# Kernel tuning notes

Measured on AMD Instinct MI355X. Metric: run time of the kernel, lower is better.

The kernel has to match this reference:

```python
import jax, jax.numpy as jnp
import numpy as np

N_PER_G = 100  # nodes per graph


def setup_inputs() -> dict:
    key = jax.random.key(0)
    ks = jax.random.split(key, 12)
    N, G, E = 100000, 1000, 1600000
    ninp, nout, K, H, H2 = 3, 10, 5, 64, 32
    x = jax.random.normal(ks[0], (N, ninp), jnp.float32)
    # within-graph random edges (contiguous node blocks per graph)
    epg = E // G
    gid = jnp.arange(E, dtype=jnp.int32) // epg
    src = jax.random.randint(ks[1], (E,), 0, N_PER_G, jnp.int32) + gid * N_PER_G
    dst = jax.random.randint(ks[2], (E,), 0, N_PER_G, jnp.int32) + gid * N_PER_G
    edge_index = jnp.stack([src, dst])
    batch = (jnp.arange(N, dtype=jnp.int32) // N_PER_G)
    lambda_max = 1.5 + 0.5 * jax.random.uniform(ks[3], (G,), jnp.float32)
    s = 0.05
    W1 = jax.random.normal(ks[4], (K, ninp, H), jnp.float32) * s
    b1 = jnp.zeros((H,), jnp.float32)
    W2 = jax.random.normal(ks[5], (K, H, H), jnp.float32) * s
    b2 = jnp.zeros((H,), jnp.float32)
    W3 = jax.random.normal(ks[6], (K, H, H), jnp.float32) * s
    b3 = jnp.zeros((H,), jnp.float32)
    bn_gamma = jnp.ones((H,), jnp.float32)
    bn_beta = jnp.zeros((H,), jnp.float32)
    bn_mean = jnp.zeros((H,), jnp.float32)
    bn_var = jnp.ones((H,), jnp.float32)
    fc1_w = jax.random.normal(ks[7], (H, H2), jnp.float32) * s
    fc1_b = jnp.zeros((H2,), jnp.float32)
    fc2_w = jax.random.normal(ks[8], (H2, nout), jnp.float32) * s
    fc2_b = jnp.zeros((nout,), jnp.float32)
    return dict(x=x, edge_index=edge_index, batch=batch, lambda_max=lambda_max,
                W1=W1, b1=b1, W2=W2, b2=b2, W3=W3, b3=b3,
                bn_gamma=bn_gamma, bn_beta=bn_beta, bn_mean=bn_mean, bn_var=bn_var,
                fc1_w=fc1_w, fc1_b=fc1_b, fc2_w=fc2_w, fc2_b=fc2_b)


def _cheb_conv(x, W, b, row, col, coef_edge, coef_loop):
    # PyG ChebConv with sym-normalized scaled Laplacian:
    # Lhat x = scatter_add(coef_edge * x[col] -> row) + coef_loop * x
    N = x.shape[0]
    def lhat(h):
        return jax.ops.segment_sum(coef_edge[:, None] * h[col], row,
                                   num_segments=N) + coef_loop[:, None] * h
    Tx0 = x
    out = Tx0 @ W[0]
    Tx1 = lhat(x)
    out = out + Tx1 @ W[1]
    for k in range(2, W.shape[0]):
        Tx2 = 2.0 * lhat(Tx1) - Tx0
        out = out + Tx2 @ W[k]
        Tx0, Tx1 = Tx1, Tx2
    return out + b


def reference(x, edge_index, batch, lambda_max,
              W1, b1, W2, b2, W3, b3,
              bn_gamma, bn_beta, bn_mean, bn_var,
              fc1_w, fc1_b, fc2_w, fc2_b):
    N = x.shape[0]
    G = lambda_max.shape[0]
    row, col = edge_index[0], edge_index[1]
    # sym Laplacian normalization, scaled by 2/lambda_max (per-graph)
    deg = jax.ops.segment_sum(jnp.ones_like(row, dtype=x.dtype), row, num_segments=N)
    dis = jnp.where(deg > 0, deg, 1.0) ** -0.5
    dis = jnp.where(deg > 0, dis, 0.0)
    lmax_e = lambda_max[batch[row]]
    coef_edge = -(2.0 / lmax_e) * dis[row] * dis[col]   # off-diagonal of Lhat
    coef_loop = 2.0 / lambda_max[batch] - 1.0           # diagonal of Lhat
    h = jax.nn.relu(_cheb_conv(x, W1, b1, row, col, coef_edge, coef_loop))
    h = jax.nn.relu(_cheb_conv(h, W2, b2, row, col, coef_edge, coef_loop))
    h = jax.nn.relu(_cheb_conv(h, W3, b3, row, col, coef_edge, coef_loop))
    # global mean pool over graphs
    sums = jax.ops.segment_sum(h, batch, num_segments=G)
    cnts = jax.ops.segment_sum(jnp.ones((N,), h.dtype), batch, num_segments=G)
    g = sums / jnp.maximum(cnts, 1.0)[:, None]
    # BatchNorm1d (eval mode, running stats), eps=1e-5
    g = (g - bn_mean) * jax.lax.rsqrt(bn_var + 1e-5) * bn_gamma + bn_beta
    g = jax.nn.relu(g @ fc1_w + fc1_b)
    return jax.nn.log_softmax(g @ fc2_w + fc2_b, axis=1)
```

## Files before the change

### kernel.cpp

```cpp
#include <hip/hip_runtime.h>

#define NPG 100
#define HF 64
#define ST 72
#define SAT 136
#define CMW 29

typedef float  f4   __attribute__((ext_vector_type(4)));
typedef float  f16v __attribute__((ext_vector_type(16)));
typedef short  bf8  __attribute__((ext_vector_type(8)));

#define SZ_TC  (HF * SAT * 2)
#define SZ_TRM (128 * ST * 2)
#define OFF_TRM (2 * SZ_TC)
#define OFF_MISC (OFF_TRM + 2 * SZ_TRM)
#define SMEM_BYTES (OFF_MISC + 1280)

#define WT_TOTAL 46080

__device__ __forceinline__ unsigned short f2bf(float f) {
    unsigned u = __float_as_uint(f);
    u += 0x7fffu + ((u >> 16) & 1u);
    return (unsigned short)(u >> 16);
}
__device__ __forceinline__ unsigned cvt_pk_bf16(float lo, float hi) {
    unsigned r;
    asm("v_cvt_pk_bf16_f32 %0, %1, %2" : "=v"(r) : "v"(lo), "v"(hi));
    return r;
}
__device__ __forceinline__ f16v zerov16() {
    f16v z;
    #pragma unroll
    for (int i = 0; i < 16; i++) z[i] = 0.f;
    return z;
}
__device__ __forceinline__ void bar_lgkm() {
    asm volatile("s_waitcnt lgkmcnt(0)" ::: "memory");
    __builtin_amdgcn_s_barrier();
    __builtin_amdgcn_sched_barrier(0);
}

union BF8U { unsigned u[4]; bf8 b; };

__global__ void wconv(const float* __restrict__ W1, const float* __restrict__ W2,
                      const float* __restrict__ W3, unsigned short* __restrict__ ws)
{
    int idx = blockIdx.x * 256 + threadIdx.x;
    if (idx >= WT_TOTAL) return;
    float v;
    if (idx < 5120) {
        int k5 = idx >> 10, rem = idx & 1023, fo = rem >> 4, fi = rem & 15;
        v = (fi < 3) ? W1[(k5 * 3 + fi) * HF + fo] : 0.f;
    } else if (idx < 25600) {
        int j = idx - 5120;
        int k5 = j >> 12, rem = j & 4095, fo = rem >> 6, fi = rem & 63;
        v = W2[(k5 * HF + fi) * HF + fo];
    } else {
        int j = idx - 25600;
        int k5 = j >> 12, rem = j & 4095, fo = rem >> 6, fi = rem & 63;
        v = W3[(k5 * HF + fi) * HF + fo];
    }
    ws[idx] = f2bf(v);
}

__launch_bounds__(256, 2)
__global__ void chebreg(const float* __restrict__ x, const int* __restrict__ ei,
                        const float* __restrict__ lambda_max,
                        const unsigned short* __restrict__ Wt,
                        const float* __restrict__ b1, const float* __restrict__ b2,
                        const float* __restrict__ b3,
                        const float* __restrict__ bng, const float* __restrict__ bnb,
                        const float* __restrict__ bnm, const float* __restrict__ bnv,
                        const float* __restrict__ fc1w, const float* __restrict__ fc1b,
                        const float* __restrict__ fc2w, const float* __restrict__ fc2b,
                        float* __restrict__ out, int E_total, int epg)
{
    extern __shared__ char sm[];
    const int tid = threadIdx.x;
    const int g = blockIdx.x;
    const int ebase = g * epg, nbase = g * NPG;
    const int wg = tid >> 6, lane = tid & 63;
    const int l31 = lane & 31, hh = lane >> 5;
    const int ht  = wg & 1;
    const int Mt0 = (wg >> 1) * 2;
    const int fo  = ht * 32 + l31;

    unsigned* Cm  = (unsigned*)sm;
    float* dis    = (float*)(sm + OFF_MISC);
    float* pool   = (float*)(sm + OFF_MISC + 448);
    float* gvn    = (float*)(sm + OFF_MISC + 704);
    float* zf     = (float*)(sm + OFF_MISC + 960);
    float* logits = (float*)(sm + OFF_MISC + 1088);
    float* lsep   = (float*)(sm + OFF_MISC + 1152);

    const float lam = lambda_max[g];
    const float two_l = 2.0f / lam;
    const float cl = two_l - 1.0f;

    for (int i = tid; i < (128 * CMW) / 4; i += 256)
        ((f4*)Cm)[i] = (f4){0.f, 0.f, 0.f, 0.f};
    bar_lgkm();
    for (int e = tid; e < epg; e += 256) {
        int r = ei[ebase + e] - nbase;
        int c = ei[E_total + ebase + e] - nbase;
        atomicAdd(&Cm[r * CMW + (c >> 2)], 1u << (8 * (c & 3)));
    }
    bar_lgkm();
    if (tid < 112) {
        float dv = 0.f;
        if (tid < NPG) {
            unsigned s = 0;
            #pragma unroll
            for (int w = 0; w < 25; w++) {
                unsigned u = Cm[tid * CMW + w];
                s += (u & 255) + ((u >> 8) & 255) + ((u >> 16) & 255) + (u >> 24);
            }
            dv = s > 0 ? rsqrtf((float)s) : 0.f;
        }
        dis[tid] = dv;
    }
    bar_lgkm();

    bf8 af[2][7];
    #pragma unroll
    for (int m = 0; m < 2; m++) {
        int rr = 32 * (Mt0 + m) + l31;
        bool rv = (rr < NPG);
        float base = rv ? (-two_l * dis[rr]) : 0.f;
        #pragma unroll
        for (int Ks = 0; Ks < 7; Ks++) {
            int k0 = Ks * 16 + 8 * hh;
            unsigned w0 = rv ? Cm[rr * CMW + (k0 >> 2)]     : 0u;
            unsigned w1 = rv ? Cm[rr * CMW + (k0 >> 2) + 1] : 0u;
            float vv[8];
            #pragma unroll
            for (int j = 0; j < 8; j++) {
                int k = k0 + j;
                unsigned cnt = (((j < 4) ? w0 : w1) >> (8 * (k & 3))) & 255u;
                float v = base * (float)cnt * dis[k];
                if (rv && k == rr) v += cl;
                vv[j] = v;
            }
            BF8U t;
            #pragma unroll
            for (int p = 0; p < 4; p++) t.u[p] = cvt_pk_bf16(vv[2 * p], vv[2 * p + 1]);
            af[m][Ks] = t.b;
        }
    }
    bar_lgkm();

    for (int i = tid; i < SZ_TC / 16; i += 256)
        ((f4*)sm)[i] = (f4){0.f, 0.f, 0.f, 0.f};
    for (int i = tid; i < SZ_TRM / 16; i += 256)
        ((f4*)(sm + OFF_TRM))[i] = (f4){0.f, 0.f, 0.f, 0.f};
    if (tid < HF) pool[tid] = 0.f;
    bar_lgkm();
    if (tid < NPG) {
        unsigned short h0 = f2bf(x[(nbase + tid) * 3 + 0]);
        unsigned short h1 = f2bf(x[(nbase + tid) * 3 + 1]);
        unsigned short h2 = f2bf(x[(nbase + tid) * 3 + 2]);
        *(unsigned*)(sm + OFF_TRM + (tid * ST) * 2) = (unsigned)h0 | ((unsigned)h1 << 16);
        *(unsigned short*)(sm + OFF_TRM + (tid * ST + 2) * 2) = h2;
        *(unsigned short*)(sm + (0 * SAT + tid) * 2) = h0;
        *(unsigned short*)(sm + (1 * SAT + tid) * 2) = h1;
        *(unsigned short*)(sm + (2 * SAT + tid) * 2) = h2;
    }
    bar_lgkm();

    f16v acc[2];
    unsigned prev[2][8], oldr[2][8];
    const float* bsv[3] = {b1, b2, b3};

    for (int L = 0; L < 3; L++) {
        const bool l1 = (L == 0);
        const unsigned short* Wl = l1 ? Wt : (Wt + (L == 1 ? 5120 : 25600));
        const int pb = L & 1;
        const float bias = bsv[L][fo];
        acc[0] = zerov16();
        acc[1] = zerov16();

        if (L == 0) {
            #pragma unroll
            for (int m = 0; m < 2; m++) {
                unsigned short tv[16];
                #pragma unroll
                for (int r = 0; r < 16; r++) {
                    int np = (Mt0 + m) * 32 + (r & 3) + 8 * (r >> 2) + 4 * hh;
                    tv[r] = *(const unsigned short*)(sm + OFF_TRM + (np * ST + fo) * 2);
                }
                #pragma unroll
                for (int p = 0; p < 8; p++)
                    prev[m][p] = (unsigned)tv[2 * p] | ((unsigned)tv[2 * p + 1] << 16);
            }
        }

        auto TW = [&](int k5, const char* trb) {
            const int nKs = l1 ? 1 : 4;
            for (int Ks = 0; Ks < nKs; Ks++) {
                bf8 bw;
                if (l1) bw = *(const bf8*)(Wl + (k5 * 64 + fo) * 16 + 8 * hh);
                else    bw = *(const bf8*)(Wl + (k5 * 64 + fo) * 64 + Ks * 16 + 8 * hh);
                #pragma unroll
                for (int m = 0; m < 2; m++) {
                    bf8 a = *(const bf8*)(trb +
                              (((Mt0 + m) * 32 + l31) * ST + Ks * 16 + 8 * hh) * 2);
                    acc[m] = __builtin_amdgcn_mfma_f32_32x32x16_bf16(a, bw, acc[m], 0, 0, 0);
                }
            }
        };

        for (int s = 1; s <= 4; s++) {
            const int rp = (pb + s - 1) & 1, wp = rp ^ 1;
            const char* tcR = sm + rp * SZ_TC;
            const char* trR = sm + OFF_TRM + rp * SZ_TRM;
            char* tcW = sm + wp * SZ_TC;
            char* trW = sm + OFF_TRM + wp * SZ_TRM;

            TW(s - 1, trR);

            bf8 bfr[7];
            #pragma unroll
            for (int Ks = 0; Ks < 7; Ks++)
                bfr[Ks] = *(const bf8*)(tcR + (fo * SAT + Ks * 16 + 8 * hh) * 2);

            #pragma unroll
            for (int m = 0; m < 2; m++) {
                f16v c = zerov16();
                #pragma unroll
                for (int Ks = 0; Ks < 7; Ks++)
                    c = __builtin_amdgcn_mfma_f32_32x32x16_bf16(af[m][Ks], bfr[Ks], c, 0, 0, 0);
                #pragma unroll
                for (int p = 0; p < 8; p++) {
                    float ve = c[2 * p], vo = c[2 * p + 1];
                    if (s >= 2) {
                        unsigned o = oldr[m][p];
                        ve = 2.f * ve - __uint_as_float(o << 16);
                        vo = 2.f * vo - __uint_as_float(o & 0xffff0000u);
                    }
                    oldr[m][p] = prev[m][p];
                    prev[m][p] = cvt_pk_bf16(ve, vo);
                }
                if (s < 4) {
                    #pragma unroll
                    for (int q4 = 0; q4 < 4; q4++) {
                        int np0 = (Mt0 + m) * 32 + 8 * q4 + 4 * hh;
                        uint2 pk;
                        pk.x = prev[m][2 * q4];
                        pk.y = prev[m][2 * q4 + 1];
                        *(uint2*)(tcW + (fo * SAT + np0) * 2) = pk;
                    }
                }
                #pragma unroll
                for (int p = 0; p < 8; p++) {
                    int r0 = 2 * p;
                    int npb = (Mt0 + m) * 32 + (r0 & 3) + 8 * (r0 >> 2) + 4 * hh;
                    char* ad = trW + (npb * ST + fo) * 2;
                    *(unsigned short*)ad = (unsigned short)prev[m][p];
                    *(unsigned short*)(ad + ST * 2) = (unsigned short)(prev[m][p] >> 16);
                }
            }
            bar_lgkm();
        }

        TW(4, sm + OFF_TRM + pb * SZ_TRM);

        if (L < 2) {
            const int op = pb ^ 1;
            char* tcW = sm + op * SZ_TC;
            char* trW = sm + OFF_TRM + op * SZ_TRM;
            #pragma unroll
            for (int m = 0; m < 2; m++) {
                #pragma unroll
                for (int p = 0; p < 8; p++) {
                    float ve = fmaxf(acc[m][2 * p]     + bias, 0.f);
                    float vo = fmaxf(acc[m][2 * p + 1] + bias, 0.f);
                    prev[m][p] = cvt_pk_bf16(ve, vo);
                }
                #pragma unroll
                for (int q4 = 0; q4 < 4; q4++) {
                    int np0 = (Mt0 + m) * 32 + 8 * q4 + 4 * hh;
                    uint2 pk;
                    pk.x = prev[m][2 * q4];
                    pk.y = prev[m][2 * q4 + 1];
                    *(uint2*)(tcW + (fo * SAT + np0) * 2) = pk;
                }
                #pragma unroll
                for (int p = 0; p < 8; p++) {
                    int r0 = 2 * p;
                    int npb = (Mt0 + m) * 32 + (r0 & 3) + 8 * (r0 >> 2) + 4 * hh;
                    char* ad = trW + (npb * ST + fo) * 2;
                    *(unsigned short*)ad = (unsigned short)prev[m][p];
                    *(unsigned short*)(ad + ST * 2) = (unsigned short)(prev[m][p] >> 16);
                }
            }
            bar_lgkm();
        } else {
            float ssum = 0.f;
            #pragma unroll
            for (int m = 0; m < 2; m++) {
                #pragma unroll
                for (int r = 0; r < 16; r++) {
                    int np = (Mt0 + m) * 32 + (r & 3) + 8 * (r >> 2) + 4 * hh;
                    float h = fmaxf(acc[m][r] + bias, 0.f);
                    if (np < NPG) ssum += h;
                }
            }
            ssum += __shfl_xor(ssum, 32, 64);
            if (hh == 0) atomicAdd(&pool[fo], ssum);
            bar_lgkm();
        }
    }

    if (tid < HF) {
        float gv = pool[tid] * (1.0f / NPG);
        gv = (gv - bnm[tid]) * rsqrtf(bnv[tid] + 1e-5f) * bng[tid] + bnb[tid];
        gvn[tid] = gv;
    }
    bar_lgkm();
    if (tid < 32) {
        float a = fc1b[tid];
        for (int f = 0; f < HF; f++) a += gvn[f] * fc1w[f * 32 + tid];
        zf[tid] = fmaxf(a, 0.f);
    }
    bar_lgkm();
    if (tid < 10) {
        float a = fc2b[tid];
        for (int k = 0; k < 32; k++) a += zf[k] * fc2w[k * 10 + tid];
        logits[tid] = a;
    }
    bar_lgkm();
    if (tid == 0) {
        float m = logits[0];
        for (int i = 1; i < 10; i++) m = fmaxf(m, logits[i]);
        float s = 0.f;
        for (int i = 0; i < 10; i++) s += expf(logits[i] - m);
        lsep[0] = m + logf(s);
    }
    bar_lgkm();
    if (tid < 10) out[g * 10 + tid] = logits[tid] - lsep[0];
}

extern "C" void kernel_launch(void* const* d_in, const int* in_sizes, int n_in,
                              void* d_out, int out_size, void* d_ws, size_t ws_size,
                              hipStream_t stream) {
    const float* x    = (const float*)d_in[0];
    const int*   ei   = (const int*)d_in[1];
    const float* lmax = (const float*)d_in[3];
    const float* W1   = (const float*)d_in[4];
    const float* b1   = (const float*)d_in[5];
    const float* W2   = (const float*)d_in[6];
    const float* b2   = (const float*)d_in[7];
    const float* W3   = (const float*)d_in[8];
    const float* b3   = (const float*)d_in[9];
    const float* bng  = (const float*)d_in[10];
    const float* bnb  = (const float*)d_in[11];
    const float* bnm  = (const float*)d_in[12];
    const float* bnv  = (const float*)d_in[13];
    const float* fc1w = (const float*)d_in[14];
    const float* fc1b = (const float*)d_in[15];
    const float* fc2w = (const float*)d_in[16];
    const float* fc2b = (const float*)d_in[17];

    const int E = in_sizes[1] / 2;
    const int G = in_sizes[3];
    const int epg = E / G;

    unsigned short* Wt = (unsigned short*)d_ws;

    wconv<<<(WT_TOTAL + 255) / 256, 256, 0, stream>>>(W1, W2, W3, Wt);

    hipFuncSetAttribute((const void*)chebreg,
                        hipFuncAttributeMaxDynamicSharedMemorySize, SMEM_BYTES);

    chebreg<<<G, 256, SMEM_BYTES, stream>>>(x, ei, lmax, Wt, b1, b2, b3,
                                            bng, bnb, bnm, bnv, fc1w, fc1b, fc2w, fc2b,
                                            (float*)d_out, E, epg);
}
```

Baseline: 159.5 us.

## Single-buffer LDS Chebyshev buffers with extra barriers to cut shared memory

Replaces the double-buffered feature tiles (column-major and row-major copies) with single buffers, which roughly halves LDS use per block. To keep reads and writes from racing, a barrier is added after the reads of each step and before the layer-output writes. The aim is more resident blocks per CU through the smaller LDS footprint, at the cost of two extra block-wide syncs per step that serialize reading and writing.

```diff
diff --git a/kernel.cpp b/kernel.cpp
--- a/kernel.cpp
+++ b/kernel.cpp
@@ -12,8 +12,8 @@
 
 #define SZ_TC  (HF * SAT * 2)
 #define SZ_TRM (128 * ST * 2)
-#define OFF_TRM (2 * SZ_TC)
-#define OFF_MISC (OFF_TRM + 2 * SZ_TRM)
+#define OFF_TRM SZ_TC
+#define OFF_MISC (OFF_TRM + SZ_TRM)
 #define SMEM_BYTES (OFF_MISC + 1280)
 
 #define WT_TOTAL 46080
@@ -149,10 +149,8 @@
     }
     bar_lgkm();
 
-    for (int i = tid; i < SZ_TC / 16; i += 256)
+    for (int i = tid; i < (SZ_TC + SZ_TRM) / 16; i += 256)
         ((f4*)sm)[i] = (f4){0.f, 0.f, 0.f, 0.f};
-    for (int i = tid; i < SZ_TRM / 16; i += 256)
-        ((f4*)(sm + OFF_TRM))[i] = (f4){0.f, 0.f, 0.f, 0.f};
     if (tid < HF) pool[tid] = 0.f;
     bar_lgkm();
     if (tid < NPG) {
@@ -174,7 +172,6 @@
     for (int L = 0; L < 3; L++) {
         const bool l1 = (L == 0);
         const unsigned short* Wl = l1 ? Wt : (Wt + (L == 1 ? 5120 : 25600));
-        const int pb = L & 1;
         const float bias = bsv[L][fo];
         acc[0] = zerov16();
         acc[1] = zerov16();
@@ -194,7 +191,7 @@
             }
         }
 
-        auto TW = [&](int k5, const char* trb) {
+        auto TW = [&](int k5) {
             const int nKs = l1 ? 1 : 4;
             for (int Ks = 0; Ks < nKs; Ks++) {
                 bf8 bw;
@@ -202,7 +199,7 @@
                 else    bw = *(const bf8*)(Wl + (k5 * 64 + fo) * 64 + Ks * 16 + 8 * hh);
                 #pragma unroll
                 for (int m = 0; m < 2; m++) {
-                    bf8 a = *(const bf8*)(trb +
+                    bf8 a = *(const bf8*)(sm + OFF_TRM +
                               (((Mt0 + m) * 32 + l31) * ST + Ks * 16 + 8 * hh) * 2);
                     acc[m] = __builtin_amdgcn_mfma_f32_32x32x16_bf16(a, bw, acc[m], 0, 0, 0);
                 }
@@ -210,18 +207,12 @@
         };
 
         for (int s = 1; s <= 4; s++) {
-            const int rp = (pb + s - 1) & 1, wp = rp ^ 1;
-            const char* tcR = sm + rp * SZ_TC;
-            const char* trR = sm + OFF_TRM + rp * SZ_TRM;
-            char* tcW = sm + wp * SZ_TC;
-            char* trW = sm + OFF_TRM + wp * SZ_TRM;
-
-            TW(s - 1, trR);
-
+            TW(s - 1);
             bf8 bfr[7];
             #pragma unroll
             for (int Ks = 0; Ks < 7; Ks++)
-                bfr[Ks] = *(const bf8*)(tcR + (fo * SAT + Ks * 16 + 8 * hh) * 2);
+                bfr[Ks] = *(const bf8*)(sm + (fo * SAT + Ks * 16 + 8 * hh) * 2);
+            bar_lgkm();
 
             #pragma unroll
             for (int m = 0; m < 2; m++) {
@@ -247,14 +238,14 @@
                         uint2 pk;
                         pk.x = prev[m][2 * q4];
                         pk.y = prev[m][2 * q4 + 1];
-                        *(uint2*)(tcW + (fo * SAT + np0) * 2) = pk;
+                        *(uint2*)(sm + (fo * SAT + np0) * 2) = pk;
                     }
                 }
                 #pragma unroll
                 for (int p = 0; p < 8; p++) {
                     int r0 = 2 * p;
                     int npb = (Mt0 + m) * 32 + (r0 & 3) + 8 * (r0 >> 2) + 4 * hh;
-                    char* ad = trW + (npb * ST + fo) * 2;
+                    char* ad = sm + OFF_TRM + (npb * ST + fo) * 2;
                     *(unsigned short*)ad = (unsigned short)prev[m][p];
                     *(unsigned short*)(ad + ST * 2) = (unsigned short)(prev[m][p] >> 16);
                 }
@@ -262,12 +253,10 @@
             bar_lgkm();
         }
 
-        TW(4, sm + OFF_TRM + pb * SZ_TRM);
+        TW(4);
 
         if (L < 2) {
-            const int op = pb ^ 1;
-            char* tcW = sm + op * SZ_TC;
-            char* trW = sm + OFF_TRM + op * SZ_TRM;
+            bar_lgkm();
             #pragma unroll
             for (int m = 0; m < 2; m++) {
                 #pragma unroll
@@ -282,13 +271,13 @@
                     uint2 pk;
                     pk.x = prev[m][2 * q4];
                     pk.y = prev[m][2 * q4 + 1];
-                    *(uint2*)(tcW + (fo * SAT + np0) * 2) = pk;
+                    *(uint2*)(sm + (fo * SAT + np0) * 2) = pk;
                 }
                 #pragma unroll
                 for (int p = 0; p < 8; p++) {
                     int r0 = 2 * p;
                     int npb = (Mt0 + m) * 32 + (r0 & 3) + 8 * (r0 >> 2) + 4 * hh;
-                    char* ad = trW + (npb * ST + fo) * 2;
+                    char* ad = sm + OFF_TRM + (npb * ST + fo) * 2;
                     *(unsigned short*)ad = (unsigned short)prev[m][p];
                     *(unsigned short*)(ad + ST * 2) = (unsigned short)(prev[m][p] >> 16);
                 }
```

After: 160.7 us. Within noise of the previous version (+0.7%).

## Cut barriers in setup, prefetch weight fragments, run epilogue in a single wave

Applied to the files above, without the earlier changes.

Moves the count matrix into the second TC buffer so that every shared-memory region can be zeroed in one pass. The x loads are issued early and their bf16 stores are done during the edge atomics. Degrees are counted with an extra atomic per edge instead of a separate reduction pass, which removes several block-wide barriers. Weight fragments for the next Chebyshev step and the next layer are loaded into registers ahead of use so global latency overlaps the MFMA work. The final MLP and softmax run in one wavefront with only waitcnt instead of block barriers. The cost is more register pressure and more LDS atomics per edge.

```diff
diff --git a/kernel.cpp b/kernel.cpp
--- a/kernel.cpp
+++ b/kernel.cpp
@@ -10,11 +10,13 @@
 typedef float  f16v __attribute__((ext_vector_type(16)));
 typedef short  bf8  __attribute__((ext_vector_type(8)));
 
-#define SZ_TC  (HF * SAT * 2)
-#define SZ_TRM (128 * ST * 2)
-#define OFF_TRM (2 * SZ_TC)
-#define OFF_MISC (OFF_TRM + 2 * SZ_TRM)
+#define SZ_TC   (HF * SAT * 2)
+#define SZ_TRM  (128 * ST * 2)
+#define OFF_TC1  SZ_TC
+#define OFF_TRM0 (2 * SZ_TC)
+#define OFF_MISC (OFF_TRM0 + 2 * SZ_TRM)
 #define SMEM_BYTES (OFF_MISC + 1280)
+#define CMBYTES (128 * CMW * 4)
 
 #define WT_TOTAL 46080
 
@@ -38,6 +40,9 @@
     asm volatile("s_waitcnt lgkmcnt(0)" ::: "memory");
     __builtin_amdgcn_s_barrier();
     __builtin_amdgcn_sched_barrier(0);
+}
+__device__ __forceinline__ void wait_lgkm() {
+    asm volatile("s_waitcnt lgkmcnt(0)" ::: "memory");
 }
 
 union BF8U { unsigned u[4]; bf8 b; };
@@ -85,86 +90,96 @@
     const int Mt0 = (wg >> 1) * 2;
     const int fo  = ht * 32 + l31;
 
-    unsigned* Cm  = (unsigned*)sm;
-    float* dis    = (float*)(sm + OFF_MISC);
-    float* pool   = (float*)(sm + OFF_MISC + 448);
-    float* gvn    = (float*)(sm + OFF_MISC + 704);
-    float* zf     = (float*)(sm + OFF_MISC + 960);
-    float* logits = (float*)(sm + OFF_MISC + 1088);
-    float* lsep   = (float*)(sm + OFF_MISC + 1152);
+    unsigned* Cm   = (unsigned*)(sm + OFF_TC1);
+    unsigned* deg  = (unsigned*)(sm + OFF_MISC);
+    float* pool    = (float*)(sm + OFF_MISC + 448);
+    float* gvn     = (float*)(sm + OFF_MISC + 704);
+    float* zf      = (float*)(sm + OFF_MISC + 960);
+    float* logits  = (float*)(sm + OFF_MISC + 1088);
+    float* lsep    = (float*)(sm + OFF_MISC + 1152);
 
     const float lam = lambda_max[g];
     const float two_l = 2.0f / lam;
     const float cl = two_l - 1.0f;
 
-    for (int i = tid; i < (128 * CMW) / 4; i += 256)
-        ((f4*)Cm)[i] = (f4){0.f, 0.f, 0.f, 0.f};
+    float xr0 = 0.f, xr1 = 0.f, xr2 = 0.f;
+    const bool tv = (tid < NPG);
+    if (tv) {
+        xr0 = x[(nbase + tid) * 3 + 0];
+        xr1 = x[(nbase + tid) * 3 + 1];
+        xr2 = x[(nbase + tid) * 3 + 2];
+    }
+
+    for (int i = tid; i < SZ_TC / 16; i += 256)
+        ((f4*)sm)[i] = (f4){0.f, 0.f, 0.f, 0.f};
+    for (int i = tid; i < CMBYTES / 16; i += 256)
+        ((f4*)(sm + OFF_TC1))[i] = (f4){0.f, 0.f, 0.f, 0.f};
+    for (int i = tid; i < SZ_TRM / 16; i += 256)
+        ((f4*)(sm + OFF_TRM0))[i] = (f4){0.f, 0.f, 0.f, 0.f};
+    if (tid < 112) deg[tid] = 0u;
+    if (tid < HF) pool[tid] = 0.f;
     bar_lgkm();
+
     for (int e = tid; e < epg; e += 256) {
         int r = ei[ebase + e] - nbase;
         int c = ei[E_total + ebase + e] - nbase;
         atomicAdd(&Cm[r * CMW + (c >> 2)], 1u << (8 * (c & 3)));
+        atomicAdd(&deg[r], 1u);
+    }
+    if (tv) {
+        unsigned short h0 = f2bf(xr0);
+        unsigned short h1 = f2bf(xr1);
+        unsigned short h2 = f2bf(xr2);
+        *(unsigned*)(sm + OFF_TRM0 + (tid * ST) * 2) = (unsigned)h0 | ((unsigned)h1 << 16);
+        *(unsigned short*)(sm + OFF_TRM0 + (tid * ST + 2) * 2) = h2;
+        *(unsigned short*)(sm + (0 * SAT + tid) * 2) = h0;
+        *(unsigned short*)(sm + (1 * SAT + tid) * 2) = h1;
+        *(unsigned short*)(sm + (2 * SAT + tid) * 2) = h2;
     }
     bar_lgkm();
-    if (tid < 112) {
-        float dv = 0.f;
-        if (tid < NPG) {
-            unsigned s = 0;
-            #pragma unroll
-            for (int w = 0; w < 25; w++) {
-                unsigned u = Cm[tid * CMW + w];
-                s += (u & 255) + ((u >> 8) & 255) + ((u >> 16) & 255) + (u >> 24);
-            }
-            dv = s > 0 ? rsqrtf((float)s) : 0.f;
-        }
-        dis[tid] = dv;
-    }
-    bar_lgkm();
 
     bf8 af[2][7];
-    #pragma unroll
-    for (int m = 0; m < 2; m++) {
-        int rr = 32 * (Mt0 + m) + l31;
-        bool rv = (rr < NPG);
-        float base = rv ? (-two_l * dis[rr]) : 0.f;
+    {
+        int rr[2]; bool rv[2]; float base[2];
+        #pragma unroll
+        for (int m = 0; m < 2; m++) {
+            rr[m] = 32 * (Mt0 + m) + l31;
+            rv[m] = (rr[m] < NPG);
+            unsigned dgr = rv[m] ? deg[rr[m]] : 0u;
+            float disr = dgr ? rsqrtf((float)dgr) : 0.f;
+            base[m] = rv[m] ? (-two_l * disr) : 0.f;
+        }
         #pragma unroll
         for (int Ks = 0; Ks < 7; Ks++) {
             int k0 = Ks * 16 + 8 * hh;
-            unsigned w0 = rv ? Cm[rr * CMW + (k0 >> 2)]     : 0u;
-            unsigned w1 = rv ? Cm[rr * CMW + (k0 >> 2) + 1] : 0u;
-            float vv[8];
+            float dv8[8];
             #pragma unroll
             for (int j = 0; j < 8; j++) {
-                int k = k0 + j;
-                unsigned cnt = (((j < 4) ? w0 : w1) >> (8 * (k & 3))) & 255u;
-                float v = base * (float)cnt * dis[k];
-                if (rv && k == rr) v += cl;
-                vv[j] = v;
-            }
-            BF8U t;
-            #pragma unroll
-            for (int p = 0; p < 4; p++) t.u[p] = cvt_pk_bf16(vv[2 * p], vv[2 * p + 1]);
-            af[m][Ks] = t.b;
-        }
-    }
-    bar_lgkm();
-
-    for (int i = tid; i < SZ_TC / 16; i += 256)
-        ((f4*)sm)[i] = (f4){0.f, 0.f, 0.f, 0.f};
-    for (int i = tid; i < SZ_TRM / 16; i += 256)
-        ((f4*)(sm + OFF_TRM))[i] = (f4){0.f, 0.f, 0.f, 0.f};
-    if (tid < HF) pool[tid] = 0.f;
-    bar_lgkm();
-    if (tid < NPG) {
-        unsigned short h0 = f2bf(x[(nbase + tid) * 3 + 0]);
-        unsigned short h1 = f2bf(x[(nbase + tid) * 3 + 1]);
-        unsigned short h2 = f2bf(x[(nbase + tid) * 3 + 2]);
-        *(unsigned*)(sm + OFF_TRM + (tid * ST) * 2) = (unsigned)h0 | ((unsigned)h1 << 16);
-        *(unsigned short*)(sm + OFF_TRM + (tid * ST + 2) * 2) = h2;
-        *(unsigned short*)(sm + (0 * SAT + tid) * 2) = h0;
-        *(unsigned short*)(sm + (1 * SAT + tid) * 2) = h1;
-        *(unsigned short*)(sm + (2 * SAT + tid) * 2) = h2;
-    }
+                unsigned dg = deg[k0 + j];
+                dv8[j] = dg ? rsqrtf((float)dg) : 0.f;
+            }
+            #pragma unroll
+            for (int m = 0; m < 2; m++) {
+                unsigned w0 = rv[m] ? Cm[rr[m] * CMW + (k0 >> 2)]     : 0u;
+                unsigned w1 = rv[m] ? Cm[rr[m] * CMW + (k0 >> 2) + 1] : 0u;
+                float vv[8];
+                #pragma unroll
+                for (int j = 0; j < 8; j++) {
+                    int k = k0 + j;
+                    unsigned cnt = (((j < 4) ? w0 : w1) >> (8 * (k & 3))) & 255u;
+                    float v = base[m] * (float)cnt * dv8[j];
+                    if (rv[m] && k == rr[m]) v += cl;
+                    vv[j] = v;
+                }
+                BF8U t;
+                #pragma unroll
+                for (int p = 0; p < 4; p++) t.u[p] = cvt_pk_bf16(vv[2 * p], vv[2 * p + 1]);
+                af[m][Ks] = t.b;
+            }
+        }
+    }
+    bf8 bwp[4];
+    bwp[0] = *(const bf8*)(Wt + fo * 16 + 8 * hh);
     bar_lgkm();
 
     f16v acc[2];
@@ -175,6 +190,7 @@
         const bool l1 = (L == 0);
         const unsigned short* Wl = l1 ? Wt : (Wt + (L == 1 ? 5120 : 25600));
         const int pb = L & 1;
+        const int nKs = l1 ? 1 : 4;
         const float bias = bsv[L][fo];
         acc[0] = zerov16();
         acc[1] = zerov16();
@@ -182,41 +198,43 @@
         if (L == 0) {
             #pragma unroll
             for (int m = 0; m < 2; m++) {
-                unsigned short tv[16];
+                unsigned short tvv[16];
                 #pragma unroll
                 for (int r = 0; r < 16; r++) {
                     int np = (Mt0 + m) * 32 + (r & 3) + 8 * (r >> 2) + 4 * hh;
-                    tv[r] = *(const unsigned short*)(sm + OFF_TRM + (np * ST + fo) * 2);
+                    tvv[r] = *(const unsigned short*)(sm + OFF_TRM0 + (np * ST + fo) * 2);
                 }
                 #pragma unroll
                 for (int p = 0; p < 8; p++)
-                    prev[m][p] = (unsigned)tv[2 * p] | ((unsigned)tv[2 * p + 1] << 16);
-            }
-        }
-
-        auto TW = [&](int k5, const char* trb) {
-            const int nKs = l1 ? 1 : 4;
-            for (int Ks = 0; Ks < nKs; Ks++) {
-                bf8 bw;
-                if (l1) bw = *(const bf8*)(Wl + (k5 * 64 + fo) * 16 + 8 * hh);
-                else    bw = *(const bf8*)(Wl + (k5 * 64 + fo) * 64 + Ks * 16 + 8 * hh);
-                #pragma unroll
-                for (int m = 0; m < 2; m++) {
-                    bf8 a = *(const bf8*)(trb +
-                              (((Mt0 + m) * 32 + l31) * ST + Ks * 16 + 8 * hh) * 2);
-                    acc[m] = __builtin_amdgcn_mfma_f32_32x32x16_bf16(a, bw, acc[m], 0, 0, 0);
-                }
-            }
-        };
+                    prev[m][p] = (unsigned)tvv[2 * p] | ((unsigned)tvv[2 * p + 1] << 16);
+            }
+        }
 
         for (int s = 1; s <= 4; s++) {
             const int rp = (pb + s - 1) & 1, wp = rp ^ 1;
             const char* tcR = sm + rp * SZ_TC;
-            const char* trR = sm + OFF_TRM + rp * SZ_TRM;
+            const char* trR = sm + OFF_TRM0 + rp * SZ_TRM;
             char* tcW = sm + wp * SZ_TC;
-            char* trW = sm + OFF_TRM + wp * SZ_TRM;
-
-            TW(s - 1, trR);
+            char* trW = sm + OFF_TRM0 + wp * SZ_TRM;
+
+            #pragma unroll
+            for (int Ks = 0; Ks < 4; Ks++) {
+                if (Ks < nKs) {
+                    #pragma unroll
+                    for (int m = 0; m < 2; m++) {
+                        bf8 a = *(const bf8*)(trR +
+                                  (((Mt0 + m) * 32 + l31) * ST + Ks * 16 + 8 * hh) * 2);
+                        acc[m] = __builtin_amdgcn_mfma_f32_32x32x16_bf16(a, bwp[Ks], acc[m], 0, 0, 0);
+                    }
+                }
+            }
+            if (l1) {
+                bwp[0] = *(const bf8*)(Wl + (s * 64 + fo) * 16 + 8 * hh);
+            } else {
+                #pragma unroll
+                for (int Ks = 0; Ks < 4; Ks++)
+                    bwp[Ks] = *(const bf8*)(Wl + (s * 64 + fo) * 64 + Ks * 16 + 8 * hh);
+            }
 
             bf8 bfr[7];
             #pragma unroll
@@ -262,12 +280,30 @@
             bar_lgkm();
         }
 
-        TW(4, sm + OFF_TRM + pb * SZ_TRM);
+        {
+            const char* trR = sm + OFF_TRM0 + pb * SZ_TRM;
+            #pragma unroll
+            for (int Ks = 0; Ks < 4; Ks++) {
+                if (Ks < nKs) {
+                    #pragma unroll
+                    for (int m = 0; m < 2; m++) {
+                        bf8 a = *(const bf8*)(trR +
+                                  (((Mt0 + m) * 32 + l31) * ST + Ks * 16 + 8 * hh) * 2);
+                        acc[m] = __builtin_amdgcn_mfma_f32_32x32x16_bf16(a, bwp[Ks], acc[m], 0, 0, 0);
+                    }
+                }
+            }
+        }
 
         if (L < 2) {
+            const unsigned short* Wn = Wt + (L == 0 ? 5120 : 25600);
+            #pragma unroll
+            for (int Ks = 0; Ks < 4; Ks++)
+                bwp[Ks] = *(const bf8*)(Wn + fo * 64 + Ks * 16 + 8 * hh);
+
             const int op = pb ^ 1;
             char* tcW = sm + op * SZ_TC;
-            char* trW = sm + OFF_TRM + op * SZ_TRM;
+            char* trW = sm + OFF_TRM0 + op * SZ_TRM;
             #pragma unroll
             for (int m = 0; m < 2; m++) {
                 #pragma unroll
@@ -311,33 +347,33 @@
         }
     }
 
-    if (tid < HF) {
-        float gv = pool[tid] * (1.0f / NPG);
-        gv = (gv - bnm[tid]) * rsqrtf(bnv[tid] + 1e-5f) * bng[tid] + bnb[tid];
-        gvn[tid] = gv;
-    }
-    bar_lgkm();
-    if (tid < 32) {
-        float a = fc1b[tid];
-        for (int f = 0; f < HF; f++) a += gvn[f] * fc1w[f * 32 + tid];
-        zf[tid] = fmaxf(a, 0.f);
-    }
-    bar_lgkm();
-    if (tid < 10) {
-        float a = fc2b[tid];
-        for (int k = 0; k < 32; k++) a += zf[k] * fc2w[k * 10 + tid];
-        logits[tid] = a;
-    }
-    bar_lgkm();
-    if (tid == 0) {
-        float m = logits[0];
-        for (int i = 1; i < 10; i++) m = fmaxf(m, logits[i]);
-        float s = 0.f;
-        for (int i = 0; i < 10; i++) s += expf(logits[i] - m);
-        lsep[0] = m + logf(s);
-    }
-    bar_lgkm();
-    if (tid < 10) out[g * 10 + tid] = logits[tid] - lsep[0];
+    if (wg == 0) {
+        float gv = pool[lane] * (1.0f / NPG);
+        gv = (gv - bnm[lane]) * rsqrtf(bnv[lane] + 1e-5f) * bng[lane] + bnb[lane];
+        gvn[lane] = gv;
+        wait_lgkm();
+        if (lane < 32) {
+            float a = fc1b[lane];
+            for (int f = 0; f < HF; f++) a += gvn[f] * fc1w[f * 32 + lane];
+            zf[lane] = fmaxf(a, 0.f);
+        }
+        wait_lgkm();
+        if (lane < 10) {
+            float a = fc2b[lane];
+            for (int k = 0; k < 32; k++) a += zf[k] * fc2w[k * 10 + lane];
+            logits[lane] = a;
+        }
+        wait_lgkm();
+        if (lane == 0) {
+            float m = logits[0];
+            for (int i = 1; i < 10; i++) m = fmaxf(m, logits[i]);
+            float s = 0.f;
+            for (int i = 0; i < 10; i++) s += expf(logits[i] - m);
+            lsep[0] = m + logf(s);
+        }
+        wait_lgkm();
+        if (lane < 10) out[g * 10 + lane] = logits[lane] - lsep[0];
+    }
 }
 
 extern "C" void kernel_launch(void* const* d_in, const int* in_sizes, int n_in,
```

New measurement: 157.5 us. About the same (-1.3%).
